# Performance work log

Hardware: AMD Instinct MI355X
Metric: run time of the kernel (lower is better)

Reference implementation:

```python
import jax, jax.numpy as jnp
import numpy as np

TOTAL = 131072   # total frames across all utterances
SEG = 256        # number of utterances
FEAT = 78        # input feature dim (hardcoded by Linear(78,1024))
HID = 1024
NCLS = 10


def _linear_params(key, fan_in, fan_out):
    # torch nn.Linear default init: U(-1/sqrt(fan_in), 1/sqrt(fan_in))
    bound = 1.0 / np.sqrt(fan_in)
    kw, kb = jax.random.split(key)
    W = jax.random.uniform(kw, (fan_in, fan_out), minval=-bound, maxval=bound, dtype=jnp.float32)
    b = jax.random.uniform(kb, (fan_out,), minval=-bound, maxval=bound, dtype=jnp.float32)
    return W, b


def setup_inputs() -> dict:
    key = jax.random.key(0)
    ks = jax.random.split(key, 8)
    # ragged lengths summing exactly to TOTAL
    rng = np.random.default_rng(0)
    raw = rng.integers(256, 768, size=SEG).astype(np.float64)
    lens = np.maximum(1, (raw * TOTAL / raw.sum()).astype(np.int64))
    lens[-1] += TOTAL - lens.sum()
    lengths = jnp.asarray(lens, dtype=jnp.int32)

    x = jax.random.normal(ks[0], (TOTAL, FEAT), dtype=jnp.float32)
    W1, b1 = _linear_params(ks[1], FEAT, HID)
    W2, b2 = _linear_params(ks[2], HID, HID)
    W3, b3 = _linear_params(ks[3], HID, HID)
    W4, b4 = _linear_params(ks[4], HID, HID)
    W5, b5 = _linear_params(ks[5], HID, 1)
    W6, b6 = _linear_params(ks[6], HID, HID)
    W7, b7 = _linear_params(ks[7], HID, NCLS)
    return dict(x=x, W1=W1, b1=b1, W2=W2, b2=b2, W3=W3, b3=b3, W4=W4, b4=b4,
                W5=W5, b5=b5, W6=W6, b6=b6, W7=W7, b7=b7, lengths=lengths)


def reference(x, W1, b1, W2, b2, W3, b3, W4, b4, W5, b5, W6, b6, W7, b7, lengths):
    h = jax.nn.relu(x @ W1 + b1)
    h = jax.nn.relu(h @ W2 + b2)
    h = jax.nn.relu(h @ W3 + b3)
    h = jax.nn.relu(h @ W4 + b4)            # [N, HID]
    scores = jax.nn.relu(h @ W5 + b5)[:, 0]  # per-frame attention logit [N]

    # per-segment softmax over frames, then weighted sum pooling (fused segment ops)
    n_seg = lengths.shape[0]
    seg = jnp.repeat(jnp.arange(n_seg, dtype=jnp.int32), lengths,
                     total_repeat_length=h.shape[0])          # [N] segment ids
    m = jax.ops.segment_max(scores, seg, num_segments=n_seg)  # stable softmax max
    e = jnp.exp(scores - m[seg])
    denom = jax.ops.segment_sum(e, seg, num_segments=n_seg)
    w = e / denom[seg]                                        # [N] softmax weights
    pooled = jax.ops.segment_sum(h * w[:, None], seg, num_segments=n_seg)  # [SEG, HID]

    out = jax.nn.relu(pooled @ W6 + b6) @ W7 + b7             # [SEG, 10]
    return out
```

## Files before the change

### kernel.cpp

```cpp
#include <hip/hip_runtime.h>
#include <hip/hip_fp16.h>

#define TOTAL 131072
#define SEGN  256
#define FEAT  78
#define FPAD  96
#define HID   1024
#define NCLS  10
#define FCHUNK 32

typedef __attribute__((ext_vector_type(8))) short short8;
typedef __attribute__((ext_vector_type(4))) float floatx4;

typedef __attribute__((address_space(1))) void gvoid_t;
typedef __attribute__((address_space(3))) void svoid_t;

__device__ __forceinline__ void async_copy16(const void* gsrc, void* ldst) {
    __builtin_amdgcn_global_load_lds((gvoid_t*)(void*)gsrc, (svoid_t*)ldst, 16, 0, 0);
}


__global__ void conv_x_slab(const float* __restrict__ x, __half* __restrict__ xb,
                            int row0, int rows) {
    int idx = blockIdx.x * 256 + threadIdx.x;
    if (idx >= rows * FPAD) return;
    int col = idx % FPAD;
    int r   = idx / FPAD;
    float v = (col < FEAT) ? x[(size_t)(row0 + r) * FEAT + col] : 0.0f;
    xb[idx] = __float2half(v);
}

__global__ void conv_wt_kernel(const float* __restrict__ W, __half* __restrict__ Wt,
                               int K, int N, int Kpad) {
    int idx = blockIdx.x * 256 + threadIdx.x;
    if (idx >= N * Kpad) return;
    int k = idx % Kpad;
    int n = idx / Kpad;
    float v = (k < K) ? W[(size_t)k * N + n] : 0.0f;
    Wt[idx] = __float2half(v);
}

__global__ void conv_w4_kernel(const float* __restrict__ W2, const float* __restrict__ W3,
                               const float* __restrict__ W4, const float* __restrict__ W6,
                               __half* __restrict__ w2t, __half* __restrict__ w3t,
                               __half* __restrict__ w4t, __half* __restrict__ w6t) {
    int idx = blockIdx.x * 256 + threadIdx.x;
    if (idx >= HID * HID) return;
    int k = idx % HID;
    int n = idx / HID;
    const float* Ws[4] = {W2, W3, W4, W6};
    __half* Ts[4] = {w2t, w3t, w4t, w6t};
    int w = blockIdx.y;
    Ts[w][idx] = __float2half(Ws[w][(size_t)k * HID + n]);
}


__global__ __launch_bounds__(256, 2)
void gemm_f16(const __half* __restrict__ A, const __half* __restrict__ Bt,
              __half* __restrict__ C, const float* __restrict__ bias,
              int M, int N, int K, int relu_flag,
              const float* __restrict__ W5g, float* __restrict__ scores_p)
{
    __shared__ __align__(16) short smem[4 * 128 * 32];
    short* lds_a0 = smem;
    short* lds_a1 = smem + 128 * 32;
    short* lds_b0 = smem + 2 * 128 * 32;
    short* lds_b1 = smem + 3 * 128 * 32;

    const int t   = threadIdx.x;
    const int nbn = N >> 7;
    const int nbm = M >> 7;
    int bm, bn;
    {
        const int b = blockIdx.x;
        if ((nbm & 7) == 0) {
            const int xcd = b & 7;
            const int j   = b >> 3;
            bm = xcd * (nbm >> 3) + j / nbn;
            bn = j % nbn;
        } else {
            bn = b % nbn;
            bm = b / nbn;
        }
    }
    const size_t m0 = (size_t)bm * 128;
    const size_t n0 = (size_t)bn * 128;
    const int wave = t >> 6, lane = t & 63;
    const int wm = (wave >> 1) << 6;
    const int wn = (wave & 1) << 6;
    const int l16 = lane & 15, q = lane >> 4;

    floatx4 acc[4][4] = {};

    const int c0 = t, c1 = t + 256;
    const __half* a0 = A  + (m0 + (size_t)(c0 >> 2)) * K + (c0 & 3) * 8;
    const __half* a1 = A  + (m0 + (size_t)(c1 >> 2)) * K + (c1 & 3) * 8;
    const __half* b0 = Bt + (n0 + (size_t)(c0 >> 2)) * K + (c0 & 3) * 8;
    const __half* b1 = Bt + (n0 + (size_t)(c1 >> 2)) * K + (c1 & 3) * 8;
    short* lA0_0 = &lds_a0[c0 * 8];
    short* lA0_1 = &lds_a0[c1 * 8];
    short* lA1_0 = &lds_a1[c0 * 8];
    short* lA1_1 = &lds_a1[c1 * 8];
    short* lB0_0 = &lds_b0[c0 * 8];
    short* lB0_1 = &lds_b0[c1 * 8];
    short* lB1_0 = &lds_b1[c0 * 8];
    short* lB1_1 = &lds_b1[c1 * 8];

    for (int k0 = 0; k0 < K; k0 += 64) {
        __syncthreads();
        async_copy16(a0 + k0, lA0_0);
        async_copy16(a1 + k0, lA0_1);
        async_copy16(b0 + k0, lB0_0);
        async_copy16(b1 + k0, lB0_1);
        async_copy16(a0 + k0 + 32, lA1_0);
        async_copy16(a1 + k0 + 32, lA1_1);
        async_copy16(b0 + k0 + 32, lB1_0);
        async_copy16(b1 + k0 + 32, lB1_1);
        __syncthreads();

        short8 af[4], bf[4];
#pragma unroll
        for (int i = 0; i < 4; ++i)
            af[i] = *(const short8*)&lds_a0[(wm + i * 16 + l16) * 32 + q * 8];
#pragma unroll
        for (int i = 0; i < 4; ++i)
            bf[i] = *(const short8*)&lds_b0[(wn + i * 16 + l16) * 32 + q * 8];
#pragma unroll
        for (int mi = 0; mi < 4; ++mi)
#pragma unroll
            for (int ni = 0; ni < 4; ++ni)
                acc[mi][ni] = __builtin_amdgcn_mfma_f32_16x16x32_f16(
                    af[mi], bf[ni], acc[mi][ni], 0, 0, 0);

#pragma unroll
        for (int i = 0; i < 4; ++i)
            af[i] = *(const short8*)&lds_a1[(wm + i * 16 + l16) * 32 + q * 8];
#pragma unroll
        for (int i = 0; i < 4; ++i)
            bf[i] = *(const short8*)&lds_b1[(wn + i * 16 + l16) * 32 + q * 8];
#pragma unroll
        for (int mi = 0; mi < 4; ++mi)
#pragma unroll
            for (int ni = 0; ni < 4; ++ni)
                acc[mi][ni] = __builtin_amdgcn_mfma_f32_16x16x32_f16(
                    af[mi], bf[ni], acc[mi][ni], 0, 0, 0);
    }

    __half* ct = (__half*)smem;
#pragma unroll
    for (int h = 0; h < 2; ++h) {
        __syncthreads();
        if (wm == h * 64) {
#pragma unroll
            for (int ni = 0; ni < 4; ++ni) {
                const int col = wn + ni * 16 + l16;
                const float bv = bias[n0 + col];
#pragma unroll
                for (int mi = 0; mi < 4; ++mi) {
                    const int r0l = mi * 16 + q * 4;
#pragma unroll
                    for (int r = 0; r < 4; ++r) {
                        float v = acc[mi][ni][r] + bv;
                        if (relu_flag) v = fmaxf(v, 0.0f);
                        ct[(r0l + r) * 128 + col] = __float2half(v);
                    }
                }
            }
        }
        __syncthreads();
#pragma unroll
        for (int it = 0; it < 4; ++it) {
            const int chunk = it * 256 + t;
            const int row = chunk >> 4;
            const int off = (chunk & 15) * 8;
            short8 v = *(const short8*)&ct[row * 128 + off];
            *(short8*)&C[(m0 + h * 64 + row) * N + n0 + off] = v;
            if (scores_p) {
                const float* wv = W5g + n0 + off;
                float p = 0.f;
#pragma unroll
                for (int j = 0; j < 8; ++j)
                    p += __half2float(((const __half*)&v)[j]) * wv[j];
#pragma unroll
                for (int o = 8; o > 0; o >>= 1) p += __shfl_down(p, o, 16);
                if (l16 == 0)
                    scores_p[(size_t)bn * M + m0 + h * 64 + row] = p;
            }
        }
    }
}


__global__ __launch_bounds__(256, 2)
void gemm_k96(const __half* __restrict__ A, const __half* __restrict__ Bt,
              __half* __restrict__ C, const float* __restrict__ bias, int M, int N)
{
    __shared__ __align__(16) short smem[2 * 128 * 96];
    short* lds_a = smem;
    short* lds_b = smem + 128 * 96;

    const int t   = threadIdx.x;
    const int nbn = N >> 7;
    const int nbm = M >> 7;
    int bm, bn;
    {
        const int b = blockIdx.x;
        if ((nbm & 7) == 0) {
            const int xcd = b & 7;
            const int j   = b >> 3;
            bm = xcd * (nbm >> 3) + j / nbn;
            bn = j % nbn;
        } else {
            bn = b % nbn;
            bm = b / nbn;
        }
    }
    const size_t m0 = (size_t)bm * 128;
    const size_t n0 = (size_t)bn * 128;
    const int wave = t >> 6, lane = t & 63;
    const int wm = (wave >> 1) << 6;
    const int wn = (wave & 1) << 6;
    const int l16 = lane & 15, q = lane >> 4;

#pragma unroll
    for (int i = 0; i < 6; ++i) {
        const int c = i * 256 + t;
        const int r = c / 12, j = c % 12;
        async_copy16(A  + (m0 + (size_t)r) * 96 + j * 8, &lds_a[c * 8]);
        async_copy16(Bt + (n0 + (size_t)r) * 96 + j * 8, &lds_b[c * 8]);
    }
    __syncthreads();

    floatx4 acc[4][4] = {};
#pragma unroll
    for (int ks = 0; ks < 3; ++ks) {
        short8 af[4], bf[4];
        const int xo = ks * 32 + q * 8;
#pragma unroll
        for (int i = 0; i < 4; ++i)
            af[i] = *(const short8*)&lds_a[(wm + i * 16 + l16) * 96 + xo];
#pragma unroll
        for (int i = 0; i < 4; ++i)
            bf[i] = *(const short8*)&lds_b[(wn + i * 16 + l16) * 96 + xo];
#pragma unroll
        for (int mi = 0; mi < 4; ++mi)
#pragma unroll
            for (int ni = 0; ni < 4; ++ni)
                acc[mi][ni] = __builtin_amdgcn_mfma_f32_16x16x32_f16(
                    af[mi], bf[ni], acc[mi][ni], 0, 0, 0);
    }

    __half* ct = (__half*)smem;
#pragma unroll
    for (int h = 0; h < 2; ++h) {
        __syncthreads();
        if (wm == h * 64) {
#pragma unroll
            for (int ni = 0; ni < 4; ++ni) {
                const int col = wn + ni * 16 + l16;
                const float bv = bias[n0 + col];
#pragma unroll
                for (int mi = 0; mi < 4; ++mi) {
                    const int r0l = mi * 16 + q * 4;
#pragma unroll
                    for (int r = 0; r < 4; ++r) {
                        float v = fmaxf(acc[mi][ni][r] + bv, 0.0f);
                        ct[(r0l + r) * 128 + col] = __float2half(v);
                    }
                }
            }
        }
        __syncthreads();
#pragma unroll
        for (int it = 0; it < 4; ++it) {
            const int chunk = it * 256 + t;
            const int row = chunk >> 4;
            const int off = (chunk & 15) * 8;
            *(short8*)&C[(m0 + h * 64 + row) * N + n0 + off] =
                *(const short8*)&ct[row * 128 + off];
        }
    }
}


__global__ void seg_offsets_kernel(const int* __restrict__ lengths, int* __restrict__ off) {
    if (blockIdx.x == 0 && threadIdx.x == 0) {
        int a = 0;
        off[0] = 0;
        for (int i = 0; i < SEGN; ++i) { a += lengths[i]; off[i + 1] = a; }
    }
}


__global__ __launch_bounds__(256)
void scorepool_kernel(const __half* __restrict__ h4, int slab_beg, int slab_rows,
                      const float* __restrict__ scores_p, const float* __restrict__ b5,
                      const int* __restrict__ segoff,
                      float* __restrict__ pooled, float* __restrict__ denom)
{
    __shared__ float e_sh[FCHUNK];
    const int t = threadIdx.x;
    const int f0 = slab_beg + blockIdx.x * FCHUNK;

    if (t < FCHUNK) {
        const int fl = f0 - slab_beg + t;
        float sc = 0.f;
#pragma unroll
        for (int b = 0; b < 8; ++b) sc += scores_p[(size_t)b * slab_rows + fl];
        sc = fmaxf(sc + b5[0], 0.0f);
        e_sh[t] = __expf(fminf(sc, 80.0f));
    }
    __syncthreads();

    const int c0 = t * 4;
    int lo = 0, hi = SEGN - 1;
    while (lo < hi) {
        int mid = (lo + hi + 1) >> 1;
        if (segoff[mid] <= f0) lo = mid; else hi = mid - 1;
    }
    int s = lo;
    int f = f0;
    const int fend = f0 + FCHUNK;
    const __half* base = h4 + (size_t)(f0 - slab_beg) * HID + c0;
    while (f < fend) {
        int send = segoff[s + 1];
        if (send > fend) send = fend;
        float a0 = 0.f, a1 = 0.f, a2 = 0.f, a3 = 0.f, es = 0.f;
        for (; f < send; ++f, base += HID) {
            float e = e_sh[f - f0];
            const __half2* r2 = (const __half2*)base;
            float2 u = __half22float2(r2[0]);
            float2 v = __half22float2(r2[1]);
            a0 += e * u.x; a1 += e * u.y; a2 += e * v.x; a3 += e * v.y;
            es += e;
        }
        float* p = pooled + (size_t)s * HID + c0;
        atomicAdd(p,     a0);
        atomicAdd(p + 1, a1);
        atomicAdd(p + 2, a2);
        atomicAdd(p + 3, a3);
        if (t == 0) atomicAdd(&denom[s], es);
        ++s;
    }
}


__global__ __launch_bounds__(256)
void finalize_pool_kernel(const float* __restrict__ pooled, const float* __restrict__ denom,
                          __half* __restrict__ poolh)
{
    int s = blockIdx.x, t = threadIdx.x;
    float inv = 1.0f / denom[s];
    for (int j = t; j < HID; j += 256)
        poolh[(size_t)s * HID + j] = __float2half(pooled[(size_t)s * HID + j] * inv);
}


__global__ void final_kernel(const __half* __restrict__ z, const float* __restrict__ W7,
                             const float* __restrict__ b7, float* __restrict__ out) {
    int s = blockIdx.x, t = threadIdx.x;
    float loc[NCLS];
#pragma unroll
    for (int c = 0; c < NCLS; ++c) loc[c] = 0.f;
    for (int k = t; k < HID; k += 256) {
        float zk = __half2float(z[(size_t)s * HID + k]);
        const float* wr = W7 + k * NCLS;
#pragma unroll
        for (int c = 0; c < NCLS; ++c) loc[c] += zk * wr[c];
    }
#pragma unroll
    for (int c = 0; c < NCLS; ++c)
#pragma unroll
        for (int o = 32; o > 0; o >>= 1) loc[c] += __shfl_down(loc[c], o);
    __shared__ float accs[NCLS];
    if (t < NCLS) accs[t] = 0.f;
    __syncthreads();
    if ((t & 63) == 0)
        for (int c = 0; c < NCLS; ++c) atomicAdd(&accs[c], loc[c]);
    __syncthreads();
    if (t < NCLS) out[s * NCLS + t] = accs[t] + b7[t];
}


extern "C" void kernel_launch(void* const* d_in, const int* in_sizes, int n_in,
                              void* d_out, int out_size, void* d_ws, size_t ws_size,
                              hipStream_t stream) {
    const float* x  = (const float*)d_in[0];
    const float* W1 = (const float*)d_in[1];
    const float* b1 = (const float*)d_in[2];
    const float* W2 = (const float*)d_in[3];
    const float* b2 = (const float*)d_in[4];
    const float* W3 = (const float*)d_in[5];
    const float* b3 = (const float*)d_in[6];
    const float* W4 = (const float*)d_in[7];
    const float* b4 = (const float*)d_in[8];
    const float* W5 = (const float*)d_in[9];
    const float* b5 = (const float*)d_in[10];
    const float* W6 = (const float*)d_in[11];
    const float* b6 = (const float*)d_in[12];
    const float* W7 = (const float*)d_in[13];
    const float* b7 = (const float*)d_in[14];
    const int* lengths = (const int*)d_in[15];
    float* out = (float*)d_out;

    char* ws = (char*)d_ws;
    size_t off = 0;
    auto take = [&](size_t bytes) -> char* {
        char* p = ws + off;
        off = (off + bytes + 255) & ~(size_t)255;
        return p;
    };
    __half* w1t   = (__half*)take((size_t)HID * FPAD * 2);
    __half* w2t   = (__half*)take((size_t)HID * HID * 2);
    __half* w3t   = (__half*)take((size_t)HID * HID * 2);
    __half* w4t   = (__half*)take((size_t)HID * HID * 2);
    __half* w6t   = (__half*)take((size_t)HID * HID * 2);
    int*    segoff = (int*)take((SEGN + 1) * 4);
    float*  pooled = (float*)take((size_t)SEGN * HID * 4);
    float*  denom  = (float*)take(SEGN * 4);
    __half* poolh  = (__half*)take((size_t)SEGN * HID * 2);
    __half* z      = (__half*)take((size_t)SEGN * HID * 2);

    int R = TOTAL;
    while (R > 1024) {
        size_t need = off + (size_t)R * FPAD * 2 + 2 * (size_t)R * HID * 2
                    + (size_t)8 * R * 4 + 4 * 256;
        if (need <= ws_size) break;
        R >>= 1;
    }
    __half* slabX    = (__half*)take((size_t)R * FPAD * 2);
    __half* slabA    = (__half*)take((size_t)R * HID * 2);
    __half* slabB    = (__half*)take((size_t)R * HID * 2);
    float*  scores_p = (float*)take((size_t)8 * R * 4);

    seg_offsets_kernel<<<1, 64, 0, stream>>>(lengths, segoff);
    hipMemsetAsync(pooled, 0, (size_t)SEGN * HID * 4, stream);
    hipMemsetAsync(denom, 0, SEGN * 4, stream);

    conv_wt_kernel<<<(HID * FPAD + 255) / 256, 256, 0, stream>>>(W1, w1t, FEAT, HID, FPAD);
    dim3 gW((HID * HID + 255) / 256, 4);
    conv_w4_kernel<<<gW, 256, 0, stream>>>(W2, W3, W4, W6, w2t, w3t, w4t, w6t);

    const int nBlocksSlab = (R / 128) * (HID / 128);
    for (int sb = 0; sb < TOTAL; sb += R) {
        conv_x_slab<<<(R * FPAD + 255) / 256, 256, 0, stream>>>(x, slabX, sb, R);
        gemm_k96<<<nBlocksSlab, 256, 0, stream>>>(slabX, w1t, slabA, b1, R, HID);
        gemm_f16<<<nBlocksSlab, 256, 0, stream>>>(slabA, w2t, slabB, b2, R, HID, HID, 1,
                                                  nullptr, nullptr);
        gemm_f16<<<nBlocksSlab, 256, 0, stream>>>(slabB, w3t, slabA, b3, R, HID, HID, 1,
                                                  nullptr, nullptr);
        gemm_f16<<<nBlocksSlab, 256, 0, stream>>>(slabA, w4t, slabB, b4, R, HID, HID, 1,
                                                  W5, scores_p);
        scorepool_kernel<<<R / FCHUNK, 256, 0, stream>>>(slabB, sb, R, scores_p, b5,
                                                         segoff, pooled, denom);
    }

    finalize_pool_kernel<<<SEGN, 256, 0, stream>>>(pooled, denom, poolh);
    const int nBlocksHead = (SEGN / 128) * (HID / 128);
    gemm_f16<<<nBlocksHead, 256, 0, stream>>>(poolh, w6t, z, b6, SEGN, HID, HID, 1,
                                              nullptr, nullptr);
    final_kernel<<<SEGN, 256, 0, stream>>>(z, W7, b7, out);
}
```

Baseline: 1.341 ms.

## Replace 128x128 hidden-layer GEMM with 256x256 four-stage pipelined MFMA kernel

Adds a gemm256 kernel with 256x256 output tiles, 512 threads and a four-stage async global-to-LDS pipeline using explicit vmcnt waits, barriers and priority hints. It also uses XOR-swizzled LDS layout and an XCD-aware block mapping, and the three 1024x1024 hidden layers now use it. The larger tile is meant to raise operand reuse and hide load latency. Score partials are now split into 4 column blocks instead of 8, so the pooling kernel sums 4 partials. The trade-off is much higher LDS use (128KB) and register pressure, which may limit occupancy.

```diff
diff --git a/kernel.cpp b/kernel.cpp
--- a/kernel.cpp
+++ b/kernel.cpp
@@ -52,6 +52,156 @@
     __half* Ts[4] = {w2t, w3t, w4t, w6t};
     int w = blockIdx.y;
     Ts[w][idx] = __float2half(Ws[w][(size_t)k * HID + n]);
+}
+
+
+#define VMCNT(n)  asm volatile("s_waitcnt vmcnt(" #n ")" ::: "memory")
+#define LGKM0     asm volatile("s_waitcnt lgkmcnt(0)" ::: "memory")
+#define SBAR      __builtin_amdgcn_s_barrier()
+
+#define STAGE_A(TT) do { short* d_ = smem + (((TT)&3)<<14); \
+    async_copy16(gA + (TT)*32, d_ + t*8); \
+    async_copy16(gA + (TT)*32 + kstr128, d_ + 4096 + t*8); } while (0)
+#define STAGE_B(TT) do { short* d_ = smem + (((TT)&3)<<14) + 8192; \
+    async_copy16(gB + (TT)*32, d_ + t*8); \
+    async_copy16(gB + (TT)*32 + kstr128, d_ + 4096 + t*8); } while (0)
+
+#define PHASE(TT, MH, STAGE_CODE) do { \
+    const short* ab_ = smem + (((TT)&3)<<14) + (MH)*2048; \
+    short8 af_[4]; \
+    _Pragma("unroll") \
+    for (int i_ = 0; i_ < 4; ++i_) af_[i_] = *(const short8*)&ab_[aoff + i_*512]; \
+    if ((MH) == 0) { \
+        const short* bb_ = smem + (((TT)&3)<<14) + 8192; \
+        _Pragma("unroll") \
+        for (int i_ = 0; i_ < 4; ++i_) bf[i_] = *(const short8*)&bb_[boff + i_*512]; \
+    } \
+    STAGE_CODE; \
+    SBAR; \
+    LGKM0; \
+    __builtin_amdgcn_sched_barrier(0); \
+    __builtin_amdgcn_s_setprio(1); \
+    _Pragma("unroll") \
+    for (int mi_ = 0; mi_ < 4; ++mi_) \
+        _Pragma("unroll") \
+        for (int ni_ = 0; ni_ < 4; ++ni_) \
+            acc[(MH)*4 + mi_][ni_] = __builtin_amdgcn_mfma_f32_16x16x32_f16( \
+                af_[mi_], bf[ni_], acc[(MH)*4 + mi_][ni_], 0, 0, 0); \
+    __builtin_amdgcn_s_setprio(0); \
+} while (0)
+
+__global__ __launch_bounds__(512, 2)
+void gemm256(const __half* __restrict__ A, const __half* __restrict__ Bt,
+             __half* __restrict__ C, const float* __restrict__ bias,
+             int M, int N, int K, int relu_flag,
+             const float* __restrict__ W5g, float* __restrict__ scores_p)
+{
+    __shared__ __align__(16) short smem[4 * 16384];
+
+    const int t   = threadIdx.x;
+    const int nbn = N >> 8;
+    const int nbm = M >> 8;
+    int bm, bn;
+    {
+        const int b = blockIdx.x;
+        if ((nbm & 7) == 0) {
+            const int xcd = b & 7;
+            const int j   = b >> 3;
+            bm = xcd * (nbm >> 3) + j / nbn;
+            bn = j % nbn;
+        } else {
+            bn = b % nbn;
+            bm = b / nbn;
+        }
+    }
+    const size_t m0 = (size_t)bm << 8;
+    const size_t n0 = (size_t)bn << 8;
+    const int wave = t >> 6, lane = t & 63;
+    const int wmb = (wave >> 2) << 7;
+    const int wnb = (wave & 3) << 6;
+    const int l16 = lane & 15, q = lane >> 4;
+    const int qa  = q ^ ((l16 >> 1) & 3);
+    const int aoff = (wmb + l16) * 32 + qa * 8;
+    const int boff = (wnb + l16) * 32 + qa * 8;
+
+    const int rr = t >> 2;
+    const int qs = ((t & 3) ^ ((t >> 3) & 3)) * 8;
+    const __half* gA = A  + (m0 + rr) * K + qs;
+    const __half* gB = Bt + (n0 + rr) * K + qs;
+    const int kstr128 = K << 7;
+
+    floatx4 acc[8][4] = {};
+    short8 bf[4];
+    const int NT = K >> 5;
+
+    STAGE_A(0); STAGE_B(0);
+    STAGE_A(1); STAGE_B(1);
+    STAGE_A(2); STAGE_B(2);
+    VMCNT(8);
+    SBAR;
+
+    int T = 0;
+    for (; T < NT - 3; ++T) {
+        PHASE(T, 0, STAGE_A(T + 3));
+        SBAR;
+        PHASE(T, 1, STAGE_B(T + 3));
+        __builtin_amdgcn_sched_barrier(0);
+        VMCNT(8);
+        SBAR;
+    }
+    PHASE(T, 0, (void)0);
+    SBAR;
+    PHASE(T, 1, (void)0);
+    VMCNT(4);
+    SBAR;
+    ++T;
+    PHASE(T, 0, (void)0);
+    SBAR;
+    PHASE(T, 1, (void)0);
+    VMCNT(0);
+    SBAR;
+    ++T;
+    PHASE(T, 0, (void)0);
+    SBAR;
+    PHASE(T, 1, (void)0);
+    __syncthreads();
+
+    __half* ct = (__half*)smem;
+#pragma unroll
+    for (int ni = 0; ni < 4; ++ni) {
+        const int col = wnb + ni * 16 + l16;
+        const float bv = bias[n0 + col];
+#pragma unroll
+        for (int mi = 0; mi < 8; ++mi) {
+            const int r0l = wmb + mi * 16 + q * 4;
+#pragma unroll
+            for (int r = 0; r < 4; ++r) {
+                float v = acc[mi][ni][r] + bv;
+                if (relu_flag) v = fmaxf(v, 0.0f);
+                ct[(r0l + r) * 256 + col] = __float2half(v);
+            }
+        }
+    }
+    __syncthreads();
+#pragma unroll
+    for (int it = 0; it < 16; ++it) {
+        const int chunk = it * 512 + t;
+        const int row = chunk >> 5;
+        const int c32 = chunk & 31;
+        short8 v = *(const short8*)&ct[row * 256 + c32 * 8];
+        *(short8*)&C[(m0 + row) * N + n0 + c32 * 8] = v;
+        if (scores_p) {
+            const float* wv = W5g + n0 + c32 * 8;
+            float p = 0.f;
+#pragma unroll
+            for (int j = 0; j < 8; ++j)
+                p += __half2float(((const __half*)&v)[j]) * wv[j];
+#pragma unroll
+            for (int o = 16; o > 0; o >>= 1) p += __shfl_down(p, o, 32);
+            if ((t & 31) == 0)
+                scores_p[(size_t)bn * M + m0 + row] = p;
+        }
+    }
 }
 
 
@@ -118,32 +268,32 @@
         async_copy16(b1 + k0 + 32, lB1_1);
         __syncthreads();
 
-        short8 af[4], bf[4];
+        short8 af[4], bfv[4];
 #pragma unroll
         for (int i = 0; i < 4; ++i)
             af[i] = *(const short8*)&lds_a0[(wm + i * 16 + l16) * 32 + q * 8];
 #pragma unroll
         for (int i = 0; i < 4; ++i)
-            bf[i] = *(const short8*)&lds_b0[(wn + i * 16 + l16) * 32 + q * 8];
+            bfv[i] = *(const short8*)&lds_b0[(wn + i * 16 + l16) * 32 + q * 8];
 #pragma unroll
         for (int mi = 0; mi < 4; ++mi)
 #pragma unroll
             for (int ni = 0; ni < 4; ++ni)
                 acc[mi][ni] = __builtin_amdgcn_mfma_f32_16x16x32_f16(
-                    af[mi], bf[ni], acc[mi][ni], 0, 0, 0);
+                    af[mi], bfv[ni], acc[mi][ni], 0, 0, 0);
 
 #pragma unroll
         for (int i = 0; i < 4; ++i)
             af[i] = *(const short8*)&lds_a1[(wm + i * 16 + l16) * 32 + q * 8];
 #pragma unroll
         for (int i = 0; i < 4; ++i)
-            bf[i] = *(const short8*)&lds_b1[(wn + i * 16 + l16) * 32 + q * 8];
+            bfv[i] = *(const short8*)&lds_b1[(wn + i * 16 + l16) * 32 + q * 8];
 #pragma unroll
         for (int mi = 0; mi < 4; ++mi)
 #pragma unroll
             for (int ni = 0; ni < 4; ++ni)
                 acc[mi][ni] = __builtin_amdgcn_mfma_f32_16x16x32_f16(
-                    af[mi], bf[ni], acc[mi][ni], 0, 0, 0);
+                    af[mi], bfv[ni], acc[mi][ni], 0, 0, 0);
     }
 
     __half* ct = (__half*)smem;
@@ -234,20 +384,20 @@
     floatx4 acc[4][4] = {};
 #pragma unroll
     for (int ks = 0; ks < 3; ++ks) {
-        short8 af[4], bf[4];
+        short8 af[4], bfv[4];
         const int xo = ks * 32 + q * 8;
 #pragma unroll
         for (int i = 0; i < 4; ++i)
             af[i] = *(const short8*)&lds_a[(wm + i * 16 + l16) * 96 + xo];
 #pragma unroll
         for (int i = 0; i < 4; ++i)
-            bf[i] = *(const short8*)&lds_b[(wn + i * 16 + l16) * 96 + xo];
+            bfv[i] = *(const short8*)&lds_b[(wn + i * 16 + l16) * 96 + xo];
 #pragma unroll
         for (int mi = 0; mi < 4; ++mi)
 #pragma unroll
             for (int ni = 0; ni < 4; ++ni)
                 acc[mi][ni] = __builtin_amdgcn_mfma_f32_16x16x32_f16(
-                    af[mi], bf[ni], acc[mi][ni], 0, 0, 0);
+                    af[mi], bfv[ni], acc[mi][ni], 0, 0, 0);
     }
 
     __half* ct = (__half*)smem;
@@ -306,7 +456,7 @@
         const int fl = f0 - slab_beg + t;
         float sc = 0.f;
 #pragma unroll
-        for (int b = 0; b < 8; ++b) sc += scores_p[(size_t)b * slab_rows + fl];
+        for (int b = 0; b < 4; ++b) sc += scores_p[(size_t)b * slab_rows + fl];
         sc = fmaxf(sc + b5[0], 0.0f);
         e_sh[t] = __expf(fminf(sc, 80.0f));
     }
@@ -442,15 +592,16 @@
     conv_w4_kernel<<<gW, 256, 0, stream>>>(W2, W3, W4, W6, w2t, w3t, w4t, w6t);
 
     const int nBlocksSlab = (R / 128) * (HID / 128);
+    const int nBlocks256  = (R / 256) * (HID / 256);
     for (int sb = 0; sb < TOTAL; sb += R) {
         conv_x_slab<<<(R * FPAD + 255) / 256, 256, 0, stream>>>(x, slabX, sb, R);
         gemm_k96<<<nBlocksSlab, 256, 0, stream>>>(slabX, w1t, slabA, b1, R, HID);
-        gemm_f16<<<nBlocksSlab, 256, 0, stream>>>(slabA, w2t, slabB, b2, R, HID, HID, 1,
-                                                  nullptr, nullptr);
-        gemm_f16<<<nBlocksSlab, 256, 0, stream>>>(slabB, w3t, slabA, b3, R, HID, HID, 1,
-                                                  nullptr, nullptr);
-        gemm_f16<<<nBlocksSlab, 256, 0, stream>>>(slabA, w4t, slabB, b4, R, HID, HID, 1,
-                                                  W5, scores_p);
+        gemm256<<<nBlocks256, 512, 0, stream>>>(slabA, w2t, slabB, b2, R, HID, HID, 1,
+                                                nullptr, nullptr);
+        gemm256<<<nBlocks256, 512, 0, stream>>>(slabB, w3t, slabA, b3, R, HID, HID, 1,
+                                                nullptr, nullptr);
+        gemm256<<<nBlocks256, 512, 0, stream>>>(slabA, w4t, slabB, b4, R, HID, HID, 1,
+                                                W5, scores_p);
         scorepool_kernel<<<R / FCHUNK, 256, 0, stream>>>(slabB, sb, R, scores_p, b5,
                                                          segoff, pooled, denom);
     }
```

After: 1.301 ms. 1.03x faster.
